# Optimization experiments

Measured on AMD Instinct MI355X. Metric: run time of the kernel, lower is better.

Reference implementation:

```python
import jax, jax.numpy as jnp
import numpy as np

K = 7            # kernel_size
PAD = 3          # (dilation*(K-1)+1)//2
SHARE = 8        # share_planes
CIN = 512; REL = 64; COUT = 512
B = 4; H = 32; W = 32
EPS = 1e-5


def _patches(x, k, pad):
    """Reflect-pad then extract kxk local windows.
    x: [B,C,H,W] -> [B, C, k*k, H*W] (row-major kernel-offset ordering,
    matching torch Unfold / SAN's Subtraction ordering)."""
    b, c, h, w = x.shape
    xp = jnp.pad(x, ((0, 0), (0, 0), (pad, pad), (pad, pad)), mode='reflect')
    pats = jnp.stack([xp[:, :, i:i + h, j:j + w]
                      for i in range(k) for j in range(k)], axis=2)
    return pats.reshape(b, c, k * k, h * w)


def setup_inputs() -> dict:
    key = jax.random.key(0)
    ks = jax.random.split(key, 16)
    n = lambda k_, shp, s=0.05: jax.random.normal(k_, shp, dtype=jnp.float32) * s
    return {
        'x': jax.random.normal(ks[0], (B, CIN, H, W), dtype=jnp.float32),
        # 1x1 query/key/value projections
        'w1': n(ks[1], (REL, CIN)), 'b1': n(ks[2], (REL,)),
        'w2': n(ks[3], (REL, CIN)), 'b2': n(ks[4], (REL,)),
        'w3': n(ks[5], (COUT, CIN)), 'b3': n(ks[6], (COUT,)),
        # conv_p: 1x1 conv on 2-channel position map
        'wp': n(ks[7], (2, 2), 0.5), 'bp': n(ks[8], (2,)),
        # conv_w: BN(rel+2) -> ReLU -> 1x1(rel+2->rel, no bias) -> BN(rel) -> ReLU -> 1x1(rel->out/share)
        'g0': jnp.ones((REL + 2,), jnp.float32), 'be0': jnp.zeros((REL + 2,), jnp.float32),
        'm0': n(ks[9], (REL + 2,), 0.1),
        'v0': jax.random.uniform(ks[10], (REL + 2,), jnp.float32, 0.5, 1.5),
        'wcw1': n(ks[11], (REL, REL + 2)),
        'g1': jnp.ones((REL,), jnp.float32), 'be1': jnp.zeros((REL,), jnp.float32),
        'm1': n(ks[12], (REL,), 0.1),
        'v1': jax.random.uniform(ks[13], (REL,), jnp.float32, 0.5, 1.5),
        'wcw2': n(ks[14], (COUT // SHARE, REL)), 'bcw2': n(ks[15], (COUT // SHARE,)),
    }


def reference(x, w1, b1, w2, b2, w3, b3, wp, bp,
              g0, be0, m0, v0, wcw1, g1, be1, m1, v1, wcw2, bcw2):
    b, c, h, w = x.shape
    hw = h * w
    conv1x1 = lambda W_, B_, t: jnp.einsum('oc,bchw->bohw', W_, t) + B_[None, :, None, None]
    bn = lambda t, g, be, m, v: ((t - m[None, :, None, None])
                                 * (g * jax.lax.rsqrt(v + EPS))[None, :, None, None]
                                 + be[None, :, None, None])

    x1 = conv1x1(w1, b1, x)   # [B,REL,H,W]
    x2 = conv1x1(w2, b2, x)   # [B,REL,H,W]
    x3 = conv1x1(w3, b3, x)   # [B,COUT,H,W]

    # position map: channel 0 = loc_w, channel 1 = loc_h (as in source)
    lw = jnp.broadcast_to(jnp.linspace(-1.0, 1.0, w)[None, :], (h, w))
    lh = jnp.broadcast_to(jnp.linspace(-1.0, 1.0, h)[:, None], (h, w))
    p = jnp.stack([lw, lh])[None].astype(x.dtype)          # [1,2,H,W]
    p = jnp.einsum('oc,bchw->bohw', wp, p) + bp[None, :, None, None]

    # Subtraction2(x1, x2): center query minus key neighbors -> [B,REL,K*K,HW]
    sub2 = x1.reshape(b, REL, 1, hw) - _patches(x2, K, PAD)
    # Subtraction(p): center minus neighbors -> [1,2,K*K,HW], repeat over batch
    subp = p.reshape(1, 2, 1, hw) - _patches(p, K, PAD)
    subp = jnp.broadcast_to(subp, (b, 2, K * K, hw))

    t = jnp.concatenate([sub2, subp], axis=1)              # [B,REL+2,K*K,HW]
    t = jax.nn.relu(bn(t, g0, be0, m0, v0))
    t = jnp.einsum('oc,bckn->bokn', wcw1, t)               # [B,REL,K*K,HW]
    t = jax.nn.relu(bn(t, g1, be1, m1, v1))
    wgt = jnp.einsum('oc,bckn->bokn', wcw2, t) + bcw2[None, :, None, None]
    wgt = jax.nn.softmax(wgt, axis=-2)                     # softmax over K*K window dim

    # Aggregation: out[b,c,n] = sum_k wgt[b, c//SHARE, k, n] * x3_patch[b,c,k,n]
    x3p = _patches(x3, K, PAD).reshape(b, COUT // SHARE, SHARE, K * K, hw)
    out = jnp.einsum('bgskn,bgkn->bgsn', x3p, wgt)
    return out.reshape(b, COUT, h, w)
```

## Files before the change

### kernel.cpp

```cpp
#include <hip/hip_runtime.h>
#include <hip/hip_bf16.h>
#include <math.h>

typedef float f32x4 __attribute__((ext_vector_type(4)));
typedef short s16x8 __attribute__((ext_vector_type(8)));
typedef short s16x4 __attribute__((ext_vector_type(4)));

#define KKW 49
#define HWTOT 1024
#define CIN 512
#define COUT 512

#define OFF_X1T 0
#define OFF_X2T 262144
#define OFF_X3T 524288
#define OFF_PM  2621440
#define OFF_A0  2623488
#define OFF_C0  2623554
#define OFF_W64 2623620
#define OFF_W65 2623684
#define OFF_C1V 2623748
#define OFF_W1B 2623812
#define OFF_W2B 2625860
#define OFF_W2F 2627908
#define OFF_WT  2629956
#define OFF_XT  2793796
#define WS_NEED_FLOATS 3842372ull

#define SWZ(bb)  ((bb) ^ ((((bb) >> 7) & 7) << 4))

#define GLD16(g, l) __builtin_amdgcn_global_load_lds( \
    (const __attribute__((address_space(1))) void*)(g), \
    (__attribute__((address_space(3))) void*)(l), 16, 0, 0)

__device__ __forceinline__ int refl(int m) {
    if (m < 0) m = -m;
    if (m > 31) m = 62 - m;
    return m;
}

__device__ __forceinline__ unsigned short fbf(float f) {
    unsigned u = __builtin_bit_cast(unsigned, f);
    unsigned r = u + 0x7fffu + ((u >> 16) & 1u);
    return (unsigned short)(r >> 16);
}

__device__ __forceinline__ unsigned pk2bf(float a, float b) {
    float2 f2; f2.x = a; f2.y = b;
    __hip_bfloat162 h = __float22bfloat162_rn(f2);
    union { __hip_bfloat162 h2; unsigned u; } cv;
    cv.h2 = h;
    return cv.u;
}

__device__ __forceinline__ float bf2f(unsigned short u) {
    unsigned v = (unsigned)u << 16;
    return __builtin_bit_cast(float, v);
}

__device__ __forceinline__ void setup_body(
        int tid,
        const float* __restrict__ wp, const float* __restrict__ bp,
        const float* __restrict__ g0, const float* __restrict__ be0,
        const float* __restrict__ m0, const float* __restrict__ v0,
        const float* __restrict__ wcw1,
        const float* __restrict__ g1, const float* __restrict__ be1,
        const float* __restrict__ m1, const float* __restrict__ v1,
        const float* __restrict__ wcw2,
        float* __restrict__ ws) {
    float* pm = ws + OFF_PM;
    for (int n = tid; n < HWTOT; n += 256) {
        int xx = n & 31, yy = n >> 5;
        float lw = -1.f + (2.f / 31.f) * xx;
        float lh = -1.f + (2.f / 31.f) * yy;
        pm[n * 2 + 0] = wp[0] * lw + wp[1] * lh + bp[0];
        pm[n * 2 + 1] = wp[2] * lw + wp[3] * lh + bp[1];
    }
    if (tid < 66) {
        float a = g0[tid] * rsqrtf(v0[tid] + 1e-5f);
        ws[OFF_A0 + tid] = a;
        ws[OFF_C0 + tid] = be0[tid] - m0[tid] * a;
    }
    if (tid < 64) {
        float a1c = g1[tid] * rsqrtf(v1[tid] + 1e-5f);
        ws[OFF_W64 + tid] = a1c * wcw1[tid * 66 + 64];
        ws[OFF_W65 + tid] = a1c * wcw1[tid * 66 + 65];
        ws[OFF_C1V + tid] = be1[tid] - m1[tid] * a1c;
    }
    unsigned short* w1b = (unsigned short*)(ws + OFF_W1B);
    unsigned short* w2f = (unsigned short*)(ws + OFF_W2F);
    for (int t = tid; t < 4096; t += 256) {
        int co = t >> 6, r = t & 63;
        float a1c = g1[co] * rsqrtf(v1[co] + 1e-5f);
        w1b[t] = fbf(a1c * wcw1[co * 66 + r]);
        int j = t & 7, idx = t >> 3;
        int ft = idx >> 6, l = idx & 63;
        int gt = ft >> 1, ks2 = ft & 1;
        int g = (l & 15) + gt * 16;
        int c2 = ks2 * 32 + (l >> 4) * 8 + j;
        w2f[t] = fbf(wcw2[g * 64 + c2]);
    }
}

__global__ void k_setup(const float* __restrict__ wp, const float* __restrict__ bp,
                        const float* __restrict__ g0, const float* __restrict__ be0,
                        const float* __restrict__ m0, const float* __restrict__ v0,
                        const float* __restrict__ wcw1,
                        const float* __restrict__ g1, const float* __restrict__ be1,
                        const float* __restrict__ m1, const float* __restrict__ v1,
                        const float* __restrict__ wcw2,
                        float* __restrict__ ws) {
    setup_body(threadIdx.x, wp, bp, g0, be0, m0, v0, wcw1, g1, be1, m1, v1, wcw2, ws);
}

__global__ __launch_bounds__(256) void k_prep(
        const float* __restrict__ x,
        const float* __restrict__ w1, const float* __restrict__ w2,
        const float* __restrict__ w3,
        const float* __restrict__ wp, const float* __restrict__ bp,
        const float* __restrict__ g0, const float* __restrict__ be0,
        const float* __restrict__ m0, const float* __restrict__ v0,
        const float* __restrict__ wcw1,
        const float* __restrict__ g1, const float* __restrict__ be1,
        const float* __restrict__ m1, const float* __restrict__ v1,
        const float* __restrict__ wcw2,
        float* __restrict__ ws) {
    int bid = blockIdx.x;
    int tid = threadIdx.x;
    if (bid == 296) {
        setup_body(tid, wp, bp, g0, be0, m0, v0, wcw1, g1, be1, m1, v1, wcw2, ws);
    } else if (bid < 40) {
        int mT = bid / 8, kT = bid % 8;
        char* dst = (char*)(ws + OFF_WT) + (mT * 8 + kT) * 16384;
#pragma unroll
        for (int it = 0; it < 4; ++it) {
            int item = it * 256 + tid;
            int m = item >> 3, k8 = item & 7;
            int mg = mT * 128 + m;
            const float* src;
            if (mg < 64) src = w1 + mg * CIN;
            else if (mg < 128) src = w2 + (mg - 64) * CIN;
            else src = w3 + (mg - 128) * CIN;
            int k0 = kT * 64 + k8 * 8;
            s16x8 h;
#pragma unroll
            for (int i = 0; i < 8; i++) h[i] = (short)fbf(src[k0 + i]);
            *(s16x8*)(dst + SWZ(m * 128 + k8 * 16)) = h;
        }
    } else {
        __shared__ float lds[64 * 129];
        int t = bid - 40;
        int b = t >> 6, nT = (t >> 3) & 7, kT = t & 7;
        const float* src = x + (b * CIN + kT * 64) * HWTOT + nT * 128;
#pragma unroll
        for (int it = 0; it < 8; ++it) {
            int item = it * 256 + tid;
            int kk = item >> 5, n4 = item & 31;
            float4 v = *(const float4*)(src + kk * HWTOT + n4 * 4);
            float* d = &lds[kk * 129 + n4 * 4];
            d[0] = v.x; d[1] = v.y; d[2] = v.z; d[3] = v.w;
        }
        __syncthreads();
        char* dst = (char*)(ws + OFF_XT) + ((b * 8 + nT) * 8 + kT) * 16384;
#pragma unroll
        for (int it = 0; it < 4; ++it) {
            int item = it * 256 + tid;
            int n = item >> 3, k8 = item & 7;
            s16x8 h;
#pragma unroll
            for (int i = 0; i < 8; i++) h[i] = (short)fbf(lds[(k8 * 8 + i) * 129 + n]);
            *(s16x8*)(dst + SWZ(n * 128 + k8 * 16)) = h;
        }
    }
}

__global__ __launch_bounds__(256) void k_projm(
        const float* __restrict__ b1, const float* __restrict__ b2,
        const float* __restrict__ b3, float* __restrict__ ws) {
    __shared__ __align__(16) char smem[32768];
    int tid = threadIdx.x, lane = tid & 63, wv = tid >> 6;
    int lidx = lane & 15, q = lane >> 4;
    int mT = blockIdx.x, nTT = blockIdx.y, b = blockIdx.z;
    const char* wtg = (const char*)(ws + OFF_WT) + (mT >> 1) * 8 * 16384 + (mT & 1) * 8192;
    const char* xtg = (const char*)(ws + OFF_XT) + (b * 8 + (nTT >> 1)) * 8 * 16384 + (nTT & 1) * 8192;

    f32x4 acc[4];
#pragma unroll
    for (int j = 0; j < 4; j++) acc[j] = (f32x4)0.f;

#define STAGE(kt, buf) do { \
        const char* ga_ = wtg + (kt) * 16384; \
        const char* gb_ = xtg + (kt) * 16384; \
        char* la_ = smem + (buf) * 16384; \
        char* lb_ = la_ + 8192; \
        _Pragma("unroll") \
        for (int c_ = 0; c_ < 2; c_++) { \
            GLD16(ga_ + c_ * 4096 + wv * 1024 + lane * 16, la_ + c_ * 4096 + wv * 1024); \
            GLD16(gb_ + c_ * 4096 + wv * 1024 + lane * 16, lb_ + c_ * 4096 + wv * 1024); \
        } \
    } while (0)

    STAGE(0, 0);
    __syncthreads();
    for (int kt = 0; kt < 8; kt++) {
        if (kt < 7) STAGE(kt + 1, (kt + 1) & 1);
        const char* la = smem + (kt & 1) * 16384;
        const char* lb = la + 8192;
#pragma unroll
        for (int ks = 0; ks < 2; ks++) {
            s16x8 af, bf[4];
            int kb = ks * 64 + q * 16;
            int arow = wv * 16 + lidx;
            af = *(const s16x8*)(la + SWZ(arow * 128 + kb));
#pragma unroll
            for (int f = 0; f < 4; f++) {
                int brow = f * 16 + lidx;
                bf[f] = *(const s16x8*)(lb + SWZ(brow * 128 + kb));
            }
#pragma unroll
            for (int nf = 0; nf < 4; nf++)
                acc[nf] = __builtin_amdgcn_mfma_f32_16x16x32_bf16(af, bf[nf], acc[nf], 0, 0, 0);
        }
        __syncthreads();
    }
#undef STAGE

    unsigned short* x1t = (unsigned short*)(ws + OFF_X1T);
    unsigned short* x2t = (unsigned short*)(ws + OFF_X2T);
    unsigned short* x3t = (unsigned short*)(ws + OFF_X3T);
    int mg = mT * 64 + wv * 16 + q * 4;
#pragma unroll
    for (int nf = 0; nf < 4; nf++) {
        int n = nTT * 64 + nf * 16 + lidx;
        float o[4];
        uint2 pk;
        if (mg < 64) {
#pragma unroll
            for (int r = 0; r < 4; r++)
                o[r] = ws[OFF_A0 + mg + r] * (acc[nf][r] + b1[mg + r]) + ws[OFF_C0 + mg + r];
            pk.x = pk2bf(o[0], o[1]); pk.y = pk2bf(o[2], o[3]);
            *(uint2*)(x1t + (size_t)(b * HWTOT + n) * 64 + mg) = pk;
        } else if (mg < 128) {
            int c = mg - 64;
#pragma unroll
            for (int r = 0; r < 4; r++)
                o[r] = ws[OFF_A0 + c + r] * (acc[nf][r] + b2[c + r]);
            pk.x = pk2bf(o[0], o[1]); pk.y = pk2bf(o[2], o[3]);
            *(uint2*)(x2t + (size_t)(b * HWTOT + n) * 64 + c) = pk;
        } else {
            int c = mg - 128;
#pragma unroll
            for (int r = 0; r < 4; r++)
                o[r] = acc[nf][r] + b3[c + r];
            pk.x = pk2bf(o[0], o[1]); pk.y = pk2bf(o[2], o[3]);
            *(uint2*)(x3t + (size_t)(b * HWTOT + n) * 512 + c) = pk;
        }
    }
}

__global__ __launch_bounds__(256) void k_proj(
        const float* __restrict__ x,
        const float* __restrict__ w1, const float* __restrict__ b1,
        const float* __restrict__ w2, const float* __restrict__ b2,
        const float* __restrict__ w3, const float* __restrict__ b3,
        float* __restrict__ ws) {
    __shared__ __align__(16) float As[64 * 17];
    __shared__ __align__(16) float Bs[16 * 64];
    int tid = threadIdx.x;
    int n0 = blockIdx.x * 64;
    int mT = blockIdx.y;
    int b = blockIdx.z;
    int mq = tid >> 4, nq = tid & 15;
    float acc[4][4];
#pragma unroll
    for (int i = 0; i < 4; i++)
#pragma unroll
        for (int j = 0; j < 4; j++) acc[i][j] = 0.f;

    for (int k0 = 0; k0 < CIN; k0 += 16) {
#pragma unroll
        for (int i = 0; i < 4; i++) {
            int t = tid + i * 256;
            int k = t & 15, m = t >> 4;
            int mg = mT * 64 + m;
            const float* Wrow;
            if (mg < 64) Wrow = w1 + mg * CIN;
            else if (mg < 128) Wrow = w2 + (mg - 64) * CIN;
            else Wrow = w3 + (mg - 128) * CIN;
            As[m * 17 + k] = Wrow[k0 + k];
        }
#pragma unroll
        for (int i = 0; i < 4; i++) {
            int t = tid + i * 256;
            int n = t & 63, k = t >> 6;
            Bs[k * 64 + n] = x[(b * CIN + k0 + k) * HWTOT + n0 + n];
        }
        __syncthreads();
#pragma unroll
        for (int k = 0; k < 16; k++) {
            float4 bv = *(const float4*)&Bs[k * 64 + nq * 4];
            float av[4];
#pragma unroll
            for (int i = 0; i < 4; i++) av[i] = As[(mq * 4 + i) * 17 + k];
#pragma unroll
            for (int i = 0; i < 4; i++) {
                acc[i][0] += av[i] * bv.x;
                acc[i][1] += av[i] * bv.y;
                acc[i][2] += av[i] * bv.z;
                acc[i][3] += av[i] * bv.w;
            }
        }
        __syncthreads();
    }
    unsigned short* x1t = (unsigned short*)(ws + OFF_X1T);
    unsigned short* x2t = (unsigned short*)(ws + OFF_X2T);
    unsigned short* x3t = (unsigned short*)(ws + OFF_X3T);
#pragma unroll
    for (int i = 0; i < 4; i++) {
        int mg = mT * 64 + mq * 4 + i;
        if (mg < 64) {
            float bias = b1[mg];
            float aa = ws[OFF_A0 + mg], cc = ws[OFF_C0 + mg];
#pragma unroll
            for (int j = 0; j < 4; j++) {
                int n = n0 + nq * 4 + j;
                x1t[(size_t)(b * HWTOT + n) * 64 + mg] = fbf(aa * (acc[i][j] + bias) + cc);
            }
        } else if (mg < 128) {
            int r = mg - 64;
            float bias = b2[r];
            float aa = ws[OFF_A0 + r];
#pragma unroll
            for (int j = 0; j < 4; j++) {
                int n = n0 + nq * 4 + j;
                x2t[(size_t)(b * HWTOT + n) * 64 + r] = fbf(aa * (acc[i][j] + bias));
            }
        } else {
            float bias = b3[mg - 128];
#pragma unroll
            for (int j = 0; j < 4; j++) {
                int n = n0 + nq * 4 + j;
                x3t[(size_t)(b * HWTOT + n) * 512 + (mg - 128)] = fbf(acc[i][j] + bias);
            }
        }
    }
}

__global__ __launch_bounds__(128, 4) void k_fused2(
        const float* __restrict__ ws, float* __restrict__ out) {
    __shared__ __align__(16) char smem[8448];

    int tid = threadIdx.x;
    int lane = tid & 63;
    int wv = tid >> 6;
    int lidx = lane & 15;
    int q = lane >> 4;

    int bid = blockIdx.x;
    int p = (bid & 7) * 512 + (bid >> 3);
    int b = p >> 10;
    int n = p & 1023;
    int y = n >> 5, x0 = n & 31;

    char* t1p = smem;
    int* nbo = (int*)(smem + 8192);

    const unsigned short* x1t = (const unsigned short*)(ws + OFF_X1T);
    const unsigned short* x2t = (const unsigned short*)(ws + OFF_X2T);
    const unsigned short* x3t = (const unsigned short*)(ws + OFF_X3T);
    const float* pm  = ws + OFF_PM;
    const unsigned short* w1b = (const unsigned short*)(ws + OFF_W1B);
    const unsigned short* w2f = (const unsigned short*)(ws + OFF_W2F);

    if (tid < 64) {
        int di = tid / 7 - 3, dj = tid % 7 - 3;
        nbo[tid] = refl(y + di) * 32 + refl(x0 + dj);
    }

    float pmn0 = pm[n * 2], pmn1 = pm[n * 2 + 1];
    float a064 = ws[OFF_A0 + 64], c064 = ws[OFF_C0 + 64];
    float a065 = ws[OFF_A0 + 65], c065 = ws[OFF_C0 + 65];
    float s64v[2], s65v[2];
    s16x8 xv[2][2];
#pragma unroll
    for (int cc = 0; cc < 2; cc++) {
        int ct = wv * 2 + cc;
        int col = lidx + 16 * ct;
        int di = col / 7 - 3, dj = col % 7 - 3;
        int nb = refl(y + di) * 32 + refl(x0 + dj);
        const unsigned short* x2r = x2t + (size_t)(b * HWTOT + nb) * 64 + q * 8;
        xv[cc][0] = *(const s16x8*)(x2r);
        xv[cc][1] = *(const s16x8*)(x2r + 32);
        float2 pmb = *(const float2*)(pm + nb * 2);
        s64v[cc] = fmaxf(fmaf(a064, pmn0 - pmb.x, c064), 0.f);
        s65v[cc] = fmaxf(fmaf(a065, pmn1 - pmb.y, c065), 0.f);
    }

    s16x8 af1[4][2];
#pragma unroll
    for (int cot = 0; cot < 4; cot++)
#pragma unroll
        for (int ks = 0; ks < 2; ks++)
            af1[cot][ks] = *(const s16x8*)(w1b + (lidx + 16 * cot) * 64 + ks * 32 + q * 8);

    const unsigned short* x1r = x1t + (size_t)(b * HWTOT + n) * 64 + q * 8;
    float x1f[2][8];
    {
        s16x8 h0 = *(const s16x8*)(x1r);
        s16x8 h1 = *(const s16x8*)(x1r + 32);
#pragma unroll
        for (int i = 0; i < 8; i++) {
            x1f[0][i] = bf2f((unsigned short)h0[i]);
            x1f[1][i] = bf2f((unsigned short)h1[i]);
        }
    }

#pragma unroll
    for (int cc = 0; cc < 2; cc++) {
        int col = lidx + 16 * (wv * 2 + cc);
        f32x4 acc1[4];
#pragma unroll
        for (int cot = 0; cot < 4; cot++) acc1[cot] = (f32x4)0.f;
#pragma unroll
        for (int ks = 0; ks < 2; ks++) {
            s16x8 v = xv[cc][ks];
            union { s16x8 v; unsigned u[4]; } bb;
#pragma unroll
            for (int w = 0; w < 4; w++)
                bb.u[w] = pk2bf(
                    fmaxf(x1f[ks][2 * w]     - bf2f((unsigned short)v[2 * w]),     0.f),
                    fmaxf(x1f[ks][2 * w + 1] - bf2f((unsigned short)v[2 * w + 1]), 0.f));
#pragma unroll
            for (int cot = 0; cot < 4; cot++)
                acc1[cot] = __builtin_amdgcn_mfma_f32_16x16x32_bf16(af1[cot][ks], bb.v, acc1[cot], 0, 0, 0);
        }
#pragma unroll
        for (int cot = 0; cot < 4; cot++) {
            f32x4 wa = *(const f32x4*)(ws + OFF_W64 + cot * 16 + q * 4);
            f32x4 wb = *(const f32x4*)(ws + OFF_W65 + cot * 16 + q * 4);
            f32x4 cw = *(const f32x4*)(ws + OFF_C1V + cot * 16 + q * 4);
            float t[4];
#pragma unroll
            for (int r = 0; r < 4; r++)
                t[r] = fmaxf(acc1[cot][r] + wa[r] * s64v[cc] + wb[r] * s65v[cc] + cw[r], 0.f);
            uint2 pk;
            pk.x = pk2bf(t[0], t[1]);
            pk.y = pk2bf(t[2], t[3]);
            int byte = col * 128 + cot * 32 + q * 8;
            *(uint2*)(t1p + SWZ(byte)) = pk;
        }
    }

    __syncthreads();

    unsigned held[2][4][2];
#pragma unroll
    for (int gg = 0; gg < 2; gg++) {
        int gt = wv * 2 + gg;
        s16x8 af2[2];
#pragma unroll
        for (int ks2 = 0; ks2 < 2; ks2++)
            af2[ks2] = *(const s16x8*)(w2f + ((gt * 2 + ks2) * 64 + lane) * 8);
        f32x4 acc2[4];
#pragma unroll
        for (int kt = 0; kt < 4; kt++) acc2[kt] = (f32x4)0.f;
#pragma unroll
        for (int kt = 0; kt < 4; kt++) {
#pragma unroll
            for (int ks2 = 0; ks2 < 2; ks2++) {
                int byte = (lidx + 16 * kt) * 128 + ks2 * 64 + q * 16;
                s16x8 a = *(const s16x8*)(t1p + SWZ(byte));
                acc2[kt] = __builtin_amdgcn_mfma_f32_16x16x32_bf16(a, af2[ks2], acc2[kt], 0, 0, 0);
            }
        }
        float mx = -1e30f;
#pragma unroll
        for (int kt = 0; kt < 3; kt++)
#pragma unroll
            for (int r = 0; r < 4; r++) mx = fmaxf(mx, acc2[kt][r]);
        if (q == 0) mx = fmaxf(mx, acc2[3][0]);
        mx = fmaxf(mx, __shfl_xor(mx, 16));
        mx = fmaxf(mx, __shfl_xor(mx, 32));
        float e[4][4];
        float sum = 0.f;
#pragma unroll
        for (int kt = 0; kt < 4; kt++)
#pragma unroll
            for (int r = 0; r < 4; r++) {
                bool valid = (kt < 3) || (q == 0 && r == 0);
                float ev = valid ? exp2f((acc2[kt][r] - mx) * 1.44269504f) : 0.f;
                e[kt][r] = ev;
                sum += ev;
            }
        sum += __shfl_xor(sum, 16);
        sum += __shfl_xor(sum, 32);
        float inv = 1.f / sum;
#pragma unroll
        for (int kt = 0; kt < 4; kt++) {
            held[gg][kt][0] = pk2bf(e[kt][0] * inv, e[kt][1] * inv);
            held[gg][kt][1] = pk2bf(e[kt][2] * inv, e[kt][3] * inv);
        }
    }

    __syncthreads();

#pragma unroll
    for (int gg = 0; gg < 2; gg++) {
        int gt = wv * 2 + gg;
#pragma unroll
        for (int kt = 0; kt < 4; kt++) {
            int byte = (lidx + 16 * gt) * 128 + kt * 32 + q * 8;
            uint2 pk;
            pk.x = held[gg][kt][0];
            pk.y = held[gg][kt][1];
            *(uint2*)(t1p + SWZ(byte)) = pk;
        }
    }

    __syncthreads();

    int lane2 = wv * 64 + lane;
    int g = lane2 >> 1;
    s16x8 wrow[7];
#pragma unroll
    for (int i = 0; i < 7; i++)
        wrow[i] = *(const s16x8*)(t1p + SWZ(g * 128 + i * 16));

    f32x4 a30 = (f32x4)0.f;
    const unsigned short* x3b = x3t + (size_t)b * HWTOT * 512 + lane2 * 4;
#pragma unroll
    for (int k = 0; k < KKW; k++) {
        int nb = nbo[k];
        float w = bf2f((unsigned short)wrow[k >> 3][k & 7]);
        s16x4 v = *(const s16x4*)(x3b + (size_t)nb * 512);
#pragma unroll
        for (int r = 0; r < 4; r++)
            a30[r] = fmaf(w, bf2f((unsigned short)v[r]), a30[r]);
    }
    float* ob = out + ((size_t)b * COUT + lane2 * 4) * HWTOT + n;
#pragma unroll
    for (int i = 0; i < 4; i++) ob[i * HWTOT] = a30[i];
}

__global__ __launch_bounds__(64, 4) void k_fused(
        const float* __restrict__ ws, float* __restrict__ out) {
    __shared__ __align__(16) char smem[8448];

    int lane = threadIdx.x;
    int lidx = lane & 15;
    int q = lane >> 4;

    int bid = blockIdx.x;
    int p = (bid & 7) * 512 + (bid >> 3);
    int b = p >> 10;
    int n = p & 1023;
    int y = n >> 5, x0 = n & 31;

    char* t1p = smem;
    int* nbo = (int*)(smem + 8192);

    const unsigned short* x1t = (const unsigned short*)(ws + OFF_X1T);
    const unsigned short* x2t = (const unsigned short*)(ws + OFF_X2T);
    const unsigned short* x3t = (const unsigned short*)(ws + OFF_X3T);
    const float* pm  = ws + OFF_PM;
    const unsigned short* w1b = (const unsigned short*)(ws + OFF_W1B);
    const unsigned short* w2f = (const unsigned short*)(ws + OFF_W2F);

    {
        int di = lane / 7 - 3, dj = lane % 7 - 3;
        nbo[lane] = refl(y + di) * 32 + refl(x0 + dj);
    }

    float pmn0 = pm[n * 2], pmn1 = pm[n * 2 + 1];
    float a064 = ws[OFF_A0 + 64], c064 = ws[OFF_C0 + 64];
    float a065 = ws[OFF_A0 + 65], c065 = ws[OFF_C0 + 65];
    float s64v[4], s65v[4];
    s16x8 xv[4][2];
#pragma unroll
    for (int ct = 0; ct < 4; ct++) {
        int col = lidx + 16 * ct;
        int di = col / 7 - 3, dj = col % 7 - 3;
        int nb = refl(y + di) * 32 + refl(x0 + dj);
        const unsigned short* x2r = x2t + (size_t)(b * HWTOT + nb) * 64 + q * 8;
        xv[ct][0] = *(const s16x8*)(x2r);
        xv[ct][1] = *(const s16x8*)(x2r + 32);
        float2 pmb = *(const float2*)(pm + nb * 2);
        s64v[ct] = fmaxf(fmaf(a064, pmn0 - pmb.x, c064), 0.f);
        s65v[ct] = fmaxf(fmaf(a065, pmn1 - pmb.y, c065), 0.f);
    }

    s16x8 af1[4][2];
#pragma unroll
    for (int cot = 0; cot < 4; cot++)
#pragma unroll
        for (int ks = 0; ks < 2; ks++)
            af1[cot][ks] = *(const s16x8*)(w1b + (lidx + 16 * cot) * 64 + ks * 32 + q * 8);

    const unsigned short* x1r = x1t + (size_t)(b * HWTOT + n) * 64 + q * 8;
    float x1f[2][8];
    {
        s16x8 h0 = *(const s16x8*)(x1r);
        s16x8 h1 = *(const s16x8*)(x1r + 32);
#pragma unroll
        for (int i = 0; i < 8; i++) {
            x1f[0][i] = bf2f((unsigned short)h0[i]);
            x1f[1][i] = bf2f((unsigned short)h1[i]);
        }
    }

#pragma unroll
    for (int ct = 0; ct < 4; ct++) {
        int col = lidx + 16 * ct;
        f32x4 acc1[4];
#pragma unroll
        for (int cot = 0; cot < 4; cot++) acc1[cot] = (f32x4)0.f;
#pragma unroll
        for (int ks = 0; ks < 2; ks++) {
            s16x8 v = xv[ct][ks];
            union { s16x8 v; unsigned u[4]; } bb;
#pragma unroll
            for (int w = 0; w < 4; w++)
                bb.u[w] = pk2bf(
                    fmaxf(x1f[ks][2 * w]     - bf2f((unsigned short)v[2 * w]),     0.f),
                    fmaxf(x1f[ks][2 * w + 1] - bf2f((unsigned short)v[2 * w + 1]), 0.f));
#pragma unroll
            for (int cot = 0; cot < 4; cot++)
                acc1[cot] = __builtin_amdgcn_mfma_f32_16x16x32_bf16(af1[cot][ks], bb.v, acc1[cot], 0, 0, 0);
        }
#pragma unroll
        for (int cot = 0; cot < 4; cot++) {
            f32x4 wa = *(const f32x4*)(ws + OFF_W64 + cot * 16 + q * 4);
            f32x4 wb = *(const f32x4*)(ws + OFF_W65 + cot * 16 + q * 4);
            f32x4 cc = *(const f32x4*)(ws + OFF_C1V + cot * 16 + q * 4);
            float t[4];
#pragma unroll
            for (int r = 0; r < 4; r++)
                t[r] = fmaxf(acc1[cot][r] + wa[r] * s64v[ct] + wb[r] * s65v[ct] + cc[r], 0.f);
            uint2 pk;
            pk.x = pk2bf(t[0], t[1]);
            pk.y = pk2bf(t[2], t[3]);
            int byte = col * 128 + cot * 32 + q * 8;
            *(uint2*)(t1p + SWZ(byte)) = pk;
        }
    }

    asm volatile("s_waitcnt lgkmcnt(0)" ::: "memory");
    __builtin_amdgcn_sched_barrier(0);

    s16x8 af2[4][2];
#pragma unroll
    for (int gt = 0; gt < 4; gt++)
#pragma unroll
        for (int ks2 = 0; ks2 < 2; ks2++)
            af2[gt][ks2] = *(const s16x8*)(w2f + ((gt * 2 + ks2) * 64 + lane) * 8);

    unsigned held[4][4][2];
#pragma unroll
    for (int gt = 0; gt < 4; gt++) {
        f32x4 acc2[4];
#pragma unroll
        for (int kt = 0; kt < 4; kt++) acc2[kt] = (f32x4)0.f;
#pragma unroll
        for (int kt = 0; kt < 4; kt++) {
#pragma unroll
            for (int ks2 = 0; ks2 < 2; ks2++) {
                int byte = (lidx + 16 * kt) * 128 + ks2 * 64 + q * 16;
                s16x8 a = *(const s16x8*)(t1p + SWZ(byte));
                acc2[kt] = __builtin_amdgcn_mfma_f32_16x16x32_bf16(a, af2[gt][ks2], acc2[kt], 0, 0, 0);
            }
        }
        float mx = -1e30f;
#pragma unroll
        for (int kt = 0; kt < 3; kt++)
#pragma unroll
            for (int r = 0; r < 4; r++) mx = fmaxf(mx, acc2[kt][r]);
        if (q == 0) mx = fmaxf(mx, acc2[3][0]);
        mx = fmaxf(mx, __shfl_xor(mx, 16));
        mx = fmaxf(mx, __shfl_xor(mx, 32));
        float e[4][4];
        float sum = 0.f;
#pragma unroll
        for (int kt = 0; kt < 4; kt++)
#pragma unroll
            for (int r = 0; r < 4; r++) {
                bool valid = (kt < 3) || (q == 0 && r == 0);
                float ev = valid ? exp2f((acc2[kt][r] - mx) * 1.44269504f) : 0.f;
                e[kt][r] = ev;
                sum += ev;
            }
        sum += __shfl_xor(sum, 16);
        sum += __shfl_xor(sum, 32);
        float inv = 1.f / sum;
#pragma unroll
        for (int kt = 0; kt < 4; kt++) {
            held[gt][kt][0] = pk2bf(e[kt][0] * inv, e[kt][1] * inv);
            held[gt][kt][1] = pk2bf(e[kt][2] * inv, e[kt][3] * inv);
        }
    }

#pragma unroll
    for (int gt = 0; gt < 4; gt++)
#pragma unroll
        for (int kt = 0; kt < 4; kt++) {
            int byte = (lidx + 16 * gt) * 128 + kt * 32 + q * 8;
            uint2 pk;
            pk.x = held[gt][kt][0];
            pk.y = held[gt][kt][1];
            *(uint2*)(t1p + SWZ(byte)) = pk;
        }

    asm volatile("s_waitcnt lgkmcnt(0)" ::: "memory");
    __builtin_amdgcn_sched_barrier(0);

    s16x8 wrow[7];
#pragma unroll
    for (int i = 0; i < 7; i++)
        wrow[i] = *(const s16x8*)(t1p + SWZ(lane * 128 + i * 16));

    f32x4 a30 = (f32x4)0.f, a31 = (f32x4)0.f;
    const unsigned short* x3b = x3t + (size_t)b * HWTOT * 512 + lane * 8;
#pragma unroll
    for (int k = 0; k < KKW; k++) {
        int nb = nbo[k];
        float w = bf2f((unsigned short)wrow[k >> 3][k & 7]);
        s16x8 v = *(const s16x8*)(x3b + (size_t)nb * 512);
#pragma unroll
        for (int r = 0; r < 4; r++) {
            a30[r] = fmaf(w, bf2f((unsigned short)v[r]), a30[r]);
            a31[r] = fmaf(w, bf2f((unsigned short)v[4 + r]), a31[r]);
        }
    }
    float* ob = out + ((size_t)b * COUT + lane * 8) * HWTOT + n;
#pragma unroll
    for (int i = 0; i < 4; i++) ob[i * HWTOT] = a30[i];
#pragma unroll
    for (int i = 0; i < 4; i++) ob[(i + 4) * HWTOT] = a31[i];
}

extern "C" void kernel_launch(void* const* d_in, const int* in_sizes, int n_in,
                              void* d_out, int out_size, void* d_ws, size_t ws_size,
                              hipStream_t stream) {
    const float* x = (const float*)d_in[0];
    const float* w1 = (const float*)d_in[1];
    const float* b1 = (const float*)d_in[2];
    const float* w2 = (const float*)d_in[3];
    const float* b2 = (const float*)d_in[4];
    const float* w3 = (const float*)d_in[5];
    const float* b3 = (const float*)d_in[6];
    const float* wp = (const float*)d_in[7];
    const float* bp = (const float*)d_in[8];
    const float* g0 = (const float*)d_in[9];
    const float* be0 = (const float*)d_in[10];
    const float* m0 = (const float*)d_in[11];
    const float* v0 = (const float*)d_in[12];
    const float* wcw1 = (const float*)d_in[13];
    const float* g1 = (const float*)d_in[14];
    const float* be1 = (const float*)d_in[15];
    const float* m1 = (const float*)d_in[16];
    const float* v1 = (const float*)d_in[17];
    const float* wcw2 = (const float*)d_in[18];
    float* ws = (float*)d_ws;
    float* out = (float*)d_out;

    if (ws_size >= WS_NEED_FLOATS * 4ull) {
        k_prep<<<297, 256, 0, stream>>>(x, w1, w2, w3, wp, bp, g0, be0, m0, v0,
                                        wcw1, g1, be1, m1, v1, wcw2, ws);
        k_projm<<<dim3(10, 16, 4), 256, 0, stream>>>(b1, b2, b3, ws);
        k_fused2<<<4096, 128, 0, stream>>>(ws, out);
    } else {
        k_setup<<<1, 256, 0, stream>>>(wp, bp, g0, be0, m0, v0, wcw1, g1, be1, m1, v1, wcw2, ws);
        k_proj<<<dim3(16, 10, 4), 256, 0, stream>>>(x, w1, b1, w2, b2, w3, b3, ws);
        k_fused<<<4096, 64, 0, stream>>>(ws, out);
    }
}
```

Baseline: 63.18 us.

## Process one pixel per wave in fused kernel, removing block barriers

The fused attention kernel now gives each of its two waves an independent pixel with a private 8 KB LDS region. Each wave does the full per-pixel pipeline (subtraction, MLP, softmax, aggregation) on its own, so the __syncthreads calls and the shared neighbor-offset table are gone. Reflected neighbor offsets are computed in registers, and the second-layer weight fragments are loaded early. The cost is twice the LDS per block, more registers per wave and longer serial work per wave, which may lower occupancy.

```diff
diff --git a/kernel.cpp b/kernel.cpp
--- a/kernel.cpp
+++ b/kernel.cpp
@@ -4,7 +4,6 @@
 
 typedef float f32x4 __attribute__((ext_vector_type(4)));
 typedef short s16x8 __attribute__((ext_vector_type(8)));
-typedef short s16x4 __attribute__((ext_vector_type(4)));
 
 #define KKW 49
 #define HWTOT 1024
@@ -346,9 +345,9 @@
     }
 }
 
-__global__ __launch_bounds__(128, 4) void k_fused2(
+__global__ __launch_bounds__(128, 4) void k_fused3(
         const float* __restrict__ ws, float* __restrict__ out) {
-    __shared__ __align__(16) char smem[8448];
+    __shared__ __align__(16) char smem[16384];
 
     int tid = threadIdx.x;
     int lane = tid & 63;
@@ -357,13 +356,12 @@
     int q = lane >> 4;
 
     int bid = blockIdx.x;
-    int p = (bid & 7) * 512 + (bid >> 3);
+    int p = ((bid & 7) * 256 + (bid >> 3)) * 2 + wv;
     int b = p >> 10;
     int n = p & 1023;
     int y = n >> 5, x0 = n & 31;
 
-    char* t1p = smem;
-    int* nbo = (int*)(smem + 8192);
+    char* t1p = smem + wv * 8192;
 
     const unsigned short* x1t = (const unsigned short*)(ws + OFF_X1T);
     const unsigned short* x2t = (const unsigned short*)(ws + OFF_X2T);
@@ -372,203 +370,11 @@
     const unsigned short* w1b = (const unsigned short*)(ws + OFF_W1B);
     const unsigned short* w2f = (const unsigned short*)(ws + OFF_W2F);
 
-    if (tid < 64) {
-        int di = tid / 7 - 3, dj = tid % 7 - 3;
-        nbo[tid] = refl(y + di) * 32 + refl(x0 + dj);
-    }
-
-    float pmn0 = pm[n * 2], pmn1 = pm[n * 2 + 1];
-    float a064 = ws[OFF_A0 + 64], c064 = ws[OFF_C0 + 64];
-    float a065 = ws[OFF_A0 + 65], c065 = ws[OFF_C0 + 65];
-    float s64v[2], s65v[2];
-    s16x8 xv[2][2];
-#pragma unroll
-    for (int cc = 0; cc < 2; cc++) {
-        int ct = wv * 2 + cc;
-        int col = lidx + 16 * ct;
-        int di = col / 7 - 3, dj = col % 7 - 3;
-        int nb = refl(y + di) * 32 + refl(x0 + dj);
-        const unsigned short* x2r = x2t + (size_t)(b * HWTOT + nb) * 64 + q * 8;
-        xv[cc][0] = *(const s16x8*)(x2r);
-        xv[cc][1] = *(const s16x8*)(x2r + 32);
-        float2 pmb = *(const float2*)(pm + nb * 2);
-        s64v[cc] = fmaxf(fmaf(a064, pmn0 - pmb.x, c064), 0.f);
-        s65v[cc] = fmaxf(fmaf(a065, pmn1 - pmb.y, c065), 0.f);
-    }
-
-    s16x8 af1[4][2];
-#pragma unroll
-    for (int cot = 0; cot < 4; cot++)
-#pragma unroll
-        for (int ks = 0; ks < 2; ks++)
-            af1[cot][ks] = *(const s16x8*)(w1b + (lidx + 16 * cot) * 64 + ks * 32 + q * 8);
-
-    const unsigned short* x1r = x1t + (size_t)(b * HWTOT + n) * 64 + q * 8;
-    float x1f[2][8];
-    {
-        s16x8 h0 = *(const s16x8*)(x1r);
-        s16x8 h1 = *(const s16x8*)(x1r + 32);
-#pragma unroll
-        for (int i = 0; i < 8; i++) {
-            x1f[0][i] = bf2f((unsigned short)h0[i]);
-            x1f[1][i] = bf2f((unsigned short)h1[i]);
-        }
-    }
-
-#pragma unroll
-    for (int cc = 0; cc < 2; cc++) {
-        int col = lidx + 16 * (wv * 2 + cc);
-        f32x4 acc1[4];
-#pragma unroll
-        for (int cot = 0; cot < 4; cot++) acc1[cot] = (f32x4)0.f;
-#pragma unroll
-        for (int ks = 0; ks < 2; ks++) {
-            s16x8 v = xv[cc][ks];
-            union { s16x8 v; unsigned u[4]; } bb;
-#pragma unroll
-            for (int w = 0; w < 4; w++)
-                bb.u[w] = pk2bf(
-                    fmaxf(x1f[ks][2 * w]     - bf2f((unsigned short)v[2 * w]),     0.f),
-                    fmaxf(x1f[ks][2 * w + 1] - bf2f((unsigned short)v[2 * w + 1]), 0.f));
-#pragma unroll
-            for (int cot = 0; cot < 4; cot++)
-                acc1[cot] = __builtin_amdgcn_mfma_f32_16x16x32_bf16(af1[cot][ks], bb.v, acc1[cot], 0, 0, 0);
-        }
-#pragma unroll
-        for (int cot = 0; cot < 4; cot++) {
-            f32x4 wa = *(const f32x4*)(ws + OFF_W64 + cot * 16 + q * 4);
-            f32x4 wb = *(const f32x4*)(ws + OFF_W65 + cot * 16 + q * 4);
-            f32x4 cw = *(const f32x4*)(ws + OFF_C1V + cot * 16 + q * 4);
-            float t[4];
-#pragma unroll
-            for (int r = 0; r < 4; r++)
-                t[r] = fmaxf(acc1[cot][r] + wa[r] * s64v[cc] + wb[r] * s65v[cc] + cw[r], 0.f);
-            uint2 pk;
-            pk.x = pk2bf(t[0], t[1]);
-            pk.y = pk2bf(t[2], t[3]);
-            int byte = col * 128 + cot * 32 + q * 8;
-            *(uint2*)(t1p + SWZ(byte)) = pk;
-        }
-    }
-
-    __syncthreads();
-
-    unsigned held[2][4][2];
-#pragma unroll
-    for (int gg = 0; gg < 2; gg++) {
-        int gt = wv * 2 + gg;
-        s16x8 af2[2];
-#pragma unroll
-        for (int ks2 = 0; ks2 < 2; ks2++)
-            af2[ks2] = *(const s16x8*)(w2f + ((gt * 2 + ks2) * 64 + lane) * 8);
-        f32x4 acc2[4];
-#pragma unroll
-        for (int kt = 0; kt < 4; kt++) acc2[kt] = (f32x4)0.f;
-#pragma unroll
-        for (int kt = 0; kt < 4; kt++) {
-#pragma unroll
-            for (int ks2 = 0; ks2 < 2; ks2++) {
-                int byte = (lidx + 16 * kt) * 128 + ks2 * 64 + q * 16;
-                s16x8 a = *(const s16x8*)(t1p + SWZ(byte));
-                acc2[kt] = __builtin_amdgcn_mfma_f32_16x16x32_bf16(a, af2[ks2], acc2[kt], 0, 0, 0);
-            }
-        }
-        float mx = -1e30f;
-#pragma unroll
-        for (int kt = 0; kt < 3; kt++)
-#pragma unroll
-            for (int r = 0; r < 4; r++) mx = fmaxf(mx, acc2[kt][r]);
-        if (q == 0) mx = fmaxf(mx, acc2[3][0]);
-        mx = fmaxf(mx, __shfl_xor(mx, 16));
-        mx = fmaxf(mx, __shfl_xor(mx, 32));
-        float e[4][4];
-        float sum = 0.f;
-#pragma unroll
-        for (int kt = 0; kt < 4; kt++)
-#pragma unroll
-            for (int r = 0; r < 4; r++) {
-                bool valid = (kt < 3) || (q == 0 && r == 0);
-                float ev = valid ? exp2f((acc2[kt][r] - mx) * 1.44269504f) : 0.f;
-                e[kt][r] = ev;
-                sum += ev;
-            }
-        sum += __shfl_xor(sum, 16);
-        sum += __shfl_xor(sum, 32);
-        float inv = 1.f / sum;
-#pragma unroll
-        for (int kt = 0; kt < 4; kt++) {
-            held[gg][kt][0] = pk2bf(e[kt][0] * inv, e[kt][1] * inv);
-            held[gg][kt][1] = pk2bf(e[kt][2] * inv, e[kt][3] * inv);
-        }
-    }
-
-    __syncthreads();
-
-#pragma unroll
-    for (int gg = 0; gg < 2; gg++) {
-        int gt = wv * 2 + gg;
-#pragma unroll
-        for (int kt = 0; kt < 4; kt++) {
-            int byte = (lidx + 16 * gt) * 128 + kt * 32 + q * 8;
-            uint2 pk;
-            pk.x = held[gg][kt][0];
-            pk.y = held[gg][kt][1];
-            *(uint2*)(t1p + SWZ(byte)) = pk;
-        }
-    }
-
-    __syncthreads();
-
-    int lane2 = wv * 64 + lane;
-    int g = lane2 >> 1;
-    s16x8 wrow[7];
-#pragma unroll
-    for (int i = 0; i < 7; i++)
-        wrow[i] = *(const s16x8*)(t1p + SWZ(g * 128 + i * 16));
-
-    f32x4 a30 = (f32x4)0.f;
-    const unsigned short* x3b = x3t + (size_t)b * HWTOT * 512 + lane2 * 4;
-#pragma unroll
-    for (int k = 0; k < KKW; k++) {
-        int nb = nbo[k];
-        float w = bf2f((unsigned short)wrow[k >> 3][k & 7]);
-        s16x4 v = *(const s16x4*)(x3b + (size_t)nb * 512);
-#pragma unroll
-        for (int r = 0; r < 4; r++)
-            a30[r] = fmaf(w, bf2f((unsigned short)v[r]), a30[r]);
-    }
-    float* ob = out + ((size_t)b * COUT + lane2 * 4) * HWTOT + n;
-#pragma unroll
-    for (int i = 0; i < 4; i++) ob[i * HWTOT] = a30[i];
-}
-
-__global__ __launch_bounds__(64, 4) void k_fused(
-        const float* __restrict__ ws, float* __restrict__ out) {
-    __shared__ __align__(16) char smem[8448];
-
-    int lane = threadIdx.x;
-    int lidx = lane & 15;
-    int q = lane >> 4;
-
-    int bid = blockIdx.x;
-    int p = (bid & 7) * 512 + (bid >> 3);
-    int b = p >> 10;
-    int n = p & 1023;
-    int y = n >> 5, x0 = n & 31;
-
-    char* t1p = smem;
-    int* nbo = (int*)(smem + 8192);
-
-    const unsigned short* x1t = (const unsigned short*)(ws + OFF_X1T);
-    const unsigned short* x2t = (const unsigned short*)(ws + OFF_X2T);
-    const unsigned short* x3t = (const unsigned short*)(ws + OFF_X3T);
-    const float* pm  = ws + OFF_PM;
-    const unsigned short* w1b = (const unsigned short*)(ws + OFF_W1B);
-    const unsigned short* w2f = (const unsigned short*)(ws + OFF_W2F);
-
-    {
-        int di = lane / 7 - 3, dj = lane % 7 - 3;
-        nbo[lane] = refl(y + di) * 32 + refl(x0 + dj);
+    int ry[7], rx[7];
+#pragma unroll
+    for (int i = 0; i < 7; i++) {
+        ry[i] = refl(y + i - 3) * 32;
+        rx[i] = refl(x0 + i - 3);
     }
 
     float pmn0 = pm[n * 2], pmn1 = pm[n * 2 + 1];
@@ -596,6 +402,13 @@
         for (int ks = 0; ks < 2; ks++)
             af1[cot][ks] = *(const s16x8*)(w1b + (lidx + 16 * cot) * 64 + ks * 32 + q * 8);
 
+    s16x8 af2[4][2];
+#pragma unroll
+    for (int gt = 0; gt < 4; gt++)
+#pragma unroll
+        for (int ks2 = 0; ks2 < 2; ks2++)
+            af2[gt][ks2] = *(const s16x8*)(w2f + ((gt * 2 + ks2) * 64 + lane) * 8);
+
     const unsigned short* x1r = x1t + (size_t)(b * HWTOT + n) * 64 + q * 8;
     float x1f[2][8];
     {
@@ -644,16 +457,6 @@
         }
     }
 
-    asm volatile("s_waitcnt lgkmcnt(0)" ::: "memory");
-    __builtin_amdgcn_sched_barrier(0);
-
-    s16x8 af2[4][2];
-#pragma unroll
-    for (int gt = 0; gt < 4; gt++)
-#pragma unroll
-        for (int ks2 = 0; ks2 < 2; ks2++)
-            af2[gt][ks2] = *(const s16x8*)(w2f + ((gt * 2 + ks2) * 64 + lane) * 8);
-
     unsigned held[4][4][2];
 #pragma unroll
     for (int gt = 0; gt < 4; gt++) {
@@ -709,8 +512,194 @@
             *(uint2*)(t1p + SWZ(byte)) = pk;
         }
 
-    asm volatile("s_waitcnt lgkmcnt(0)" ::: "memory");
-    __builtin_amdgcn_sched_barrier(0);
+    s16x8 wrow[7];
+#pragma unroll
+    for (int i = 0; i < 7; i++)
+        wrow[i] = *(const s16x8*)(t1p + SWZ(lane * 128 + i * 16));
+
+    f32x4 a30 = (f32x4)0.f, a31 = (f32x4)0.f;
+    const unsigned short* x3b = x3t + (size_t)b * HWTOT * 512 + lane * 8;
+#pragma unroll
+    for (int k = 0; k < KKW; k++) {
+        int nb = ry[k / 7] + rx[k % 7];
+        float w = bf2f((unsigned short)wrow[k >> 3][k & 7]);
+        s16x8 v = *(const s16x8*)(x3b + (size_t)nb * 512);
+#pragma unroll
+        for (int r = 0; r < 4; r++) {
+            a30[r] = fmaf(w, bf2f((unsigned short)v[r]), a30[r]);
+            a31[r] = fmaf(w, bf2f((unsigned short)v[4 + r]), a31[r]);
+        }
+    }
+    float* ob = out + ((size_t)b * COUT + lane * 8) * HWTOT + n;
+#pragma unroll
+    for (int i = 0; i < 4; i++) ob[i * HWTOT] = a30[i];
+#pragma unroll
+    for (int i = 0; i < 4; i++) ob[(i + 4) * HWTOT] = a31[i];
+}
+
+__global__ __launch_bounds__(64, 4) void k_fused(
+        const float* __restrict__ ws, float* __restrict__ out) {
+    __shared__ __align__(16) char smem[8448];
+
+    int lane = threadIdx.x;
+    int lidx = lane & 15;
+    int q = lane >> 4;
+
+    int bid = blockIdx.x;
+    int p = (bid & 7) * 512 + (bid >> 3);
+    int b = p >> 10;
+    int n = p & 1023;
+    int y = n >> 5, x0 = n & 31;
+
+    char* t1p = smem;
+    int* nbo = (int*)(smem + 8192);
+
+    const unsigned short* x1t = (const unsigned short*)(ws + OFF_X1T);
+    const unsigned short* x2t = (const unsigned short*)(ws + OFF_X2T);
+    const unsigned short* x3t = (const unsigned short*)(ws + OFF_X3T);
+    const float* pm  = ws + OFF_PM;
+    const unsigned short* w1b = (const unsigned short*)(ws + OFF_W1B);
+    const unsigned short* w2f = (const unsigned short*)(ws + OFF_W2F);
+
+    {
+        int di = lane / 7 - 3, dj = lane % 7 - 3;
+        nbo[lane] = refl(y + di) * 32 + refl(x0 + dj);
+    }
+
+    float pmn0 = pm[n * 2], pmn1 = pm[n * 2 + 1];
+    float a064 = ws[OFF_A0 + 64], c064 = ws[OFF_C0 + 64];
+    float a065 = ws[OFF_A0 + 65], c065 = ws[OFF_C0 + 65];
+    float s64v[4], s65v[4];
+    s16x8 xv[4][2];
+#pragma unroll
+    for (int ct = 0; ct < 4; ct++) {
+        int col = lidx + 16 * ct;
+        int di = col / 7 - 3, dj = col % 7 - 3;
+        int nb = refl(y + di) * 32 + refl(x0 + dj);
+        const unsigned short* x2r = x2t + (size_t)(b * HWTOT + nb) * 64 + q * 8;
+        xv[ct][0] = *(const s16x8*)(x2r);
+        xv[ct][1] = *(const s16x8*)(x2r + 32);
+        float2 pmb = *(const float2*)(pm + nb * 2);
+        s64v[ct] = fmaxf(fmaf(a064, pmn0 - pmb.x, c064), 0.f);
+        s65v[ct] = fmaxf(fmaf(a065, pmn1 - pmb.y, c065), 0.f);
+    }
+
+    s16x8 af1[4][2];
+#pragma unroll
+    for (int cot = 0; cot < 4; cot++)
+#pragma unroll
+        for (int ks = 0; ks < 2; ks++)
+            af1[cot][ks] = *(const s16x8*)(w1b + (lidx + 16 * cot) * 64 + ks * 32 + q * 8);
+
+    s16x8 af2[4][2];
+#pragma unroll
+    for (int gt = 0; gt < 4; gt++)
+#pragma unroll
+        for (int ks2 = 0; ks2 < 2; ks2++)
+            af2[gt][ks2] = *(const s16x8*)(w2f + ((gt * 2 + ks2) * 64 + lane) * 8);
+
+    const unsigned short* x1r = x1t + (size_t)(b * HWTOT + n) * 64 + q * 8;
+    float x1f[2][8];
+    {
+        s16x8 h0 = *(const s16x8*)(x1r);
+        s16x8 h1 = *(const s16x8*)(x1r + 32);
+#pragma unroll
+        for (int i = 0; i < 8; i++) {
+            x1f[0][i] = bf2f((unsigned short)h0[i]);
+            x1f[1][i] = bf2f((unsigned short)h1[i]);
+        }
+    }
+
+#pragma unroll
+    for (int ct = 0; ct < 4; ct++) {
+        int col = lidx + 16 * ct;
+        f32x4 acc1[4];
+#pragma unroll
+        for (int cot = 0; cot < 4; cot++) acc1[cot] = (f32x4)0.f;
+#pragma unroll
+        for (int ks = 0; ks < 2; ks++) {
+            s16x8 v = xv[ct][ks];
+            union { s16x8 v; unsigned u[4]; } bb;
+#pragma unroll
+            for (int w = 0; w < 4; w++)
+                bb.u[w] = pk2bf(
+                    fmaxf(x1f[ks][2 * w]     - bf2f((unsigned short)v[2 * w]),     0.f),
+                    fmaxf(x1f[ks][2 * w + 1] - bf2f((unsigned short)v[2 * w + 1]), 0.f));
+#pragma unroll
+            for (int cot = 0; cot < 4; cot++)
+                acc1[cot] = __builtin_amdgcn_mfma_f32_16x16x32_bf16(af1[cot][ks], bb.v, acc1[cot], 0, 0, 0);
+        }
+#pragma unroll
+        for (int cot = 0; cot < 4; cot++) {
+            f32x4 wa = *(const f32x4*)(ws + OFF_W64 + cot * 16 + q * 4);
+            f32x4 wb = *(const f32x4*)(ws + OFF_W65 + cot * 16 + q * 4);
+            f32x4 cc = *(const f32x4*)(ws + OFF_C1V + cot * 16 + q * 4);
+            float t[4];
+#pragma unroll
+            for (int r = 0; r < 4; r++)
+                t[r] = fmaxf(acc1[cot][r] + wa[r] * s64v[ct] + wb[r] * s65v[ct] + cc[r], 0.f);
+            uint2 pk;
+            pk.x = pk2bf(t[0], t[1]);
+            pk.y = pk2bf(t[2], t[3]);
+            int byte = col * 128 + cot * 32 + q * 8;
+            *(uint2*)(t1p + SWZ(byte)) = pk;
+        }
+    }
+
+    unsigned held[4][4][2];
+#pragma unroll
+    for (int gt = 0; gt < 4; gt++) {
+        f32x4 acc2[4];
+#pragma unroll
+        for (int kt = 0; kt < 4; kt++) acc2[kt] = (f32x4)0.f;
+#pragma unroll
+        for (int kt = 0; kt < 4; kt++) {
+#pragma unroll
+            for (int ks2 = 0; ks2 < 2; ks2++) {
+                int byte = (lidx + 16 * kt) * 128 + ks2 * 64 + q * 16;
+                s16x8 a = *(const s16x8*)(t1p + SWZ(byte));
+                acc2[kt] = __builtin_amdgcn_mfma_f32_16x16x32_bf16(a, af2[gt][ks2], acc2[kt], 0, 0, 0);
+            }
+        }
+        float mx = -1e30f;
+#pragma unroll
+        for (int kt = 0; kt < 3; kt++)
+#pragma unroll
+            for (int r = 0; r < 4; r++) mx = fmaxf(mx, acc2[kt][r]);
+        if (q == 0) mx = fmaxf(mx, acc2[3][0]);
+        mx = fmaxf(mx, __shfl_xor(mx, 16));
+        mx = fmaxf(mx, __shfl_xor(mx, 32));
+        float e[4][4];
+        float sum = 0.f;
+#pragma unroll
+        for (int kt = 0; kt < 4; kt++)
+#pragma unroll
+            for (int r = 0; r < 4; r++) {
+                bool valid = (kt < 3) || (q == 0 && r == 0);
+                float ev = valid ? exp2f((acc2[kt][r] - mx) * 1.44269504f) : 0.f;
+                e[kt][r] = ev;
+                sum += ev;
+            }
+        sum += __shfl_xor(sum, 16);
+        sum += __shfl_xor(sum, 32);
+        float inv = 1.f / sum;
+#pragma unroll
+        for (int kt = 0; kt < 4; kt++) {
+            held[gt][kt][0] = pk2bf(e[kt][0] * inv, e[kt][1] * inv);
+            held[gt][kt][1] = pk2bf(e[kt][2] * inv, e[kt][3] * inv);
+        }
+    }
+
+#pragma unroll
+    for (int gt = 0; gt < 4; gt++)
+#pragma unroll
+        for (int kt = 0; kt < 4; kt++) {
+            int byte = (lidx + 16 * gt) * 128 + kt * 32 + q * 8;
+            uint2 pk;
+            pk.x = held[gt][kt][0];
+            pk.y = held[gt][kt][1];
+            *(uint2*)(t1p + SWZ(byte)) = pk;
+        }
 
     s16x8 wrow[7];
 #pragma unroll
@@ -766,7 +755,7 @@
         k_prep<<<297, 256, 0, stream>>>(x, w1, w2, w3, wp, bp, g0, be0, m0, v0,
                                         wcw1, g1, be1, m1, v1, wcw2, ws);
         k_projm<<<dim3(10, 16, 4), 256, 0, stream>>>(b1, b2, b3, ws);
-        k_fused2<<<4096, 128, 0, stream>>>(ws, out);
+        k_fused3<<<2048, 128, 0, stream>>>(ws, out);
     } else {
         k_setup<<<1, 256, 0, stream>>>(wp, bp, g0, be0, m0, v0, wcw1, g1, be1, m1, v1, wcw2, ws);
         k_proj<<<dim3(16, 10, 4), 256, 0, stream>>>(x, w1, b1, w2, b2, w3, b3, ws);
```

New measurement: 57.26 us. 9.4% less time.
